# Kernel tuning notes

Measured on AMD Instinct MI355X. Metric: run time of the kernel, lower is better.

Reference implementation:

```python
import jax, jax.numpy as jnp
import numpy as np

B, NQ, N, D, H, R = 8, 64, 257, 768, 6, 64
DH = D // H  # 128
ALL_Q_MID = NQ * R  # 4096
LN_EPS = 1e-5


def setup_inputs() -> dict:
    key = jax.random.key(0)
    ks = jax.random.split(key, 7)
    s = 0.02
    return {
        "x": jax.random.normal(ks[0], (B, NQ, D), jnp.float32),
        "context": jax.random.normal(ks[1], (B, N, D), jnp.float32),
        "Wq": jax.random.normal(ks[2], (D, D), jnp.float32) * s,
        "Wk": jax.random.normal(ks[3], (D, D), jnp.float32) * s,
        "Wv1": jax.random.normal(ks[4], (ALL_Q_MID, D), jnp.float32) * s,
        "ln_g": jnp.ones((ALL_Q_MID,), jnp.float32),
        "ln_b": jnp.zeros((ALL_Q_MID,), jnp.float32),
        "Wconv": jax.random.normal(ks[5], (NQ, D, R), jnp.float32) * s,
        "Wout": jax.random.normal(ks[6], (D, D), jnp.float32) * s,
    }


def reference(x, context, Wq, Wk, Wv1, ln_g, ln_b, Wconv, Wout):
    b, nq, d = x.shape
    n = context.shape[1]
    dh = d // H

    # q, k projections, split heads: (b, h, len, dh)
    q = (x @ Wq.T).reshape(b, nq, H, dh).transpose(0, 2, 1, 3)
    k = (context @ Wk.T).reshape(b, n, H, dh).transpose(0, 2, 1, 3)

    # q-aware V: Linear -> LayerNorm(all_q_mid) -> grouped 1x1 conv (per-query lora expand)
    mid = context @ Wv1.T                                   # (b, n, NQ*R)
    mu = mid.mean(-1, keepdims=True)
    var = mid.var(-1, keepdims=True)
    mid = (mid - mu) * jax.lax.rsqrt(var + LN_EPS) * ln_g + ln_b
    midq = mid.reshape(b, n, NQ, -1)                        # (b, n, Q, r)
    v = jnp.einsum('bnqr,qdr->bqnd', midq, Wconv)           # per-query V: (b, Q, n, d)
    v = v.reshape(b, NQ, n, H, dh).transpose(0, 3, 1, 2, 4)  # (b, h, Q, n, dh)

    scale = dh ** (-0.25)
    sim = jnp.einsum('bhid,bhjd->bhij', q * scale, k * scale)  # (b, h, Q, n)
    attn = jax.nn.softmax(sim, axis=-1)
    # per-query value aggregation: attn[i, j] pairs with v[i, j, :]
    out = jnp.einsum('bhij,bhijd->bhid', attn, v)           # (b, h, Q, dh)
    out = out.transpose(0, 2, 1, 3).reshape(b, nq, d)       # (b, Q, d)
    return out @ Wout.T
```

## Files before the change

### kernel.cpp

```cpp
#include <hip/hip_runtime.h>

#define DEV __device__ __forceinline__

typedef __attribute__((ext_vector_type(8))) short sv8;
typedef __attribute__((ext_vector_type(4))) short sv4;
typedef __attribute__((ext_vector_type(4))) float f32x4;

DEV short f2bf(float f) {
  unsigned u = __float_as_uint(f);
  unsigned r = (u + 0x7fffu + ((u >> 16) & 1u)) >> 16;
  return (short)r;
}
DEV float bf2f(short s) {
  return __uint_as_float(((unsigned)(unsigned short)s) << 16);
}

DEV void gload16(const void* g, void* l) {
  __builtin_amdgcn_global_load_lds((const __attribute__((address_space(1))) void*)g,
                                   (__attribute__((address_space(3))) void*)l, 16, 0, 0);
}

__global__ __launch_bounds__(256) void fill_zero(float* __restrict__ p, int n4) {
  int i = blockIdx.x * 256 + threadIdx.x;
  if (i < n4) ((float4*)p)[i] = make_float4(0.f, 0.f, 0.f, 0.f);
}

struct CvtArgs {
  const float* s0; const float* s1; const float* s2;
  const float* s3; const float* s4; const float* s5;
  short* d0; short* d1; short* d2; short* d3; short* d4; short* d5;
  int e0, e1, e2, e3, e4, e5;
};
__global__ __launch_bounds__(256) void cvt_all(CvtArgs a) {
  int i = blockIdx.x * 256 + threadIdx.x;
  if (i >= a.e5) return;
  const float* s; short* d; int base;
  if      (i < a.e0) { s = a.s0; d = a.d0; base = 0; }
  else if (i < a.e1) { s = a.s1; d = a.d1; base = a.e0; }
  else if (i < a.e2) { s = a.s2; d = a.d2; base = a.e1; }
  else if (i < a.e3) { s = a.s3; d = a.d3; base = a.e2; }
  else if (i < a.e4) { s = a.s4; d = a.d4; base = a.e3; }
  else               { s = a.s5; d = a.d5; base = a.e4; }
  int j = i - base;
  float4 v = ((const float4*)s)[j];
  sv4 o = { f2bf(v.x), f2bf(v.y), f2bf(v.z), f2bf(v.w) };
  ((sv4*)d)[j] = o;
}

template <int MODE, int SPLITK>
DEV void gemm_tile(const short* __restrict__ A, const short* __restrict__ B,
                   void* __restrict__ C, int M, int N, int K,
                   int bm, int bn, int ks) {
  __shared__ __align__(16) short As[2][4096];
  __shared__ __align__(16) short Bs[2][4096];
  const int tid = threadIdx.x;
  const int wave = tid >> 6, lane = tid & 63;
  const int wr = wave >> 1, wc = wave & 1;
  const int row0 = bm * 128, col0 = bn * 128;
  const int rsel = lane & 15;
  const int Am = M - 1, Bm = N - 1;
  const int lr = lane >> 2;
  const int c8 = ((lane & 3) ^ ((lane >> 2) & 3)) * 8;
  const int Ksl = K / SPLITK;
  const int kbase = ks * Ksl;
  const int nt = Ksl / 32;

  const f32x4 z = {0.f, 0.f, 0.f, 0.f};
  f32x4 acc[4][4];
#pragma unroll
  for (int m = 0; m < 4; ++m)
#pragma unroll
    for (int n = 0; n < 4; ++n) acc[m][n] = z;

  auto stage = [&](int t, int buf) {
    int k0 = kbase + t * 32;
#pragma unroll
    for (int s = 0; s < 2; ++s) {
      int chunk = s * 4 + wave;
      int rr = chunk * 16 + lr;
      int gr = row0 + rr; if (gr > Am) gr = Am;
      gload16(A + (size_t)gr * K + k0 + c8, &As[buf][chunk * 512]);
      int gc = col0 + rr; if (gc > Bm) gc = Bm;
      gload16(B + (size_t)gc * K + k0 + c8, &Bs[buf][chunk * 512]);
    }
  };

  stage(0, 0);
  __syncthreads();
  const int ko = (((lane >> 4) ^ (rsel & 3)) * 8);

  for (int t = 0; t < nt; ++t) {
    int cur = t & 1;
    if (t + 1 < nt) stage(t + 1, cur ^ 1);
    sv8 a[4], b[4];
#pragma unroll
    for (int m = 0; m < 4; ++m)
      a[m] = *(const sv8*)(&As[cur][(wr * 64 + m * 16 + rsel) * 32 + ko]);
#pragma unroll
    for (int n = 0; n < 4; ++n)
      b[n] = *(const sv8*)(&Bs[cur][(wc * 64 + n * 16 + rsel) * 32 + ko]);
#pragma unroll
    for (int m = 0; m < 4; ++m)
#pragma unroll
      for (int n = 0; n < 4; ++n)
        acc[m][n] = __builtin_amdgcn_mfma_f32_16x16x32_bf16(a[m], b[n], acc[m][n], 0, 0, 0);
    __syncthreads();
  }

  const int cc = lane & 15, cr = (lane >> 4) * 4;
#pragma unroll
  for (int m = 0; m < 4; ++m)
#pragma unroll
    for (int n = 0; n < 4; ++n) {
      int c = col0 + wc * 64 + n * 16 + cc;
#pragma unroll
      for (int j = 0; j < 4; ++j) {
        int r = row0 + wr * 64 + m * 16 + cr + j;
        if (r < M && c < N) {
          float v = acc[m][n][j];
          if (MODE == 1)      ((short*)C)[(size_t)r * N + c] = f2bf(v);
          else if (MODE == 0) ((float*)C)[(size_t)r * N + c] = v;
          else                atomicAdd(&((float*)C)[(size_t)r * N + c], v);
        }
      }
    }
}

struct GSeg { const short* A; const short* B; short* C; int M; int nb; int blk0; };
__global__ __launch_bounds__(256) void gemm3(GSeg g0, GSeg g1, GSeg g2) {
  int bid = blockIdx.x;
  GSeg g;
  if (bid < g1.blk0) g = g0;
  else if (bid < g2.blk0) g = g1;
  else g = g2;
  int local = bid - g.blk0;
  int bm = local / g.nb, bn = local % g.nb;
  gemm_tile<1, 1>(g.A, g.B, g.C, g.M, g.nb * 128, 768, bm, bn, 0);
}

__global__ __launch_bounds__(256) void gemm_out_k(const short* __restrict__ A,
                                                  const short* __restrict__ B,
                                                  float* __restrict__ C) {
  gemm_tile<2, 4>(A, B, C, 512, 768, 768, blockIdx.x, blockIdx.y, blockIdx.z);
}

DEV void ln_body(int row, short* __restrict__ mid, const float* __restrict__ g,
                 const float* __restrict__ bb, float* rs, float* rss) {
  short* p = mid + (size_t)row * 4096;
  const int tid = threadIdx.x;
  sv8 v0 = *(const sv8*)(p + tid * 16);
  sv8 v1 = *(const sv8*)(p + tid * 16 + 8);
  float x[16];
#pragma unroll
  for (int j = 0; j < 8; ++j) { x[j] = bf2f(v0[j]); x[8 + j] = bf2f(v1[j]); }
  float s = 0.f, ss = 0.f;
#pragma unroll
  for (int j = 0; j < 16; ++j) { s += x[j]; ss += x[j] * x[j]; }
#pragma unroll
  for (int off = 32; off; off >>= 1) { s += __shfl_xor(s, off); ss += __shfl_xor(ss, off); }
  if ((tid & 63) == 0) { rs[tid >> 6] = s; rss[tid >> 6] = ss; }
  __syncthreads();
  float S = rs[0] + rs[1] + rs[2] + rs[3];
  float SS = rss[0] + rss[1] + rss[2] + rss[3];
  const float inv_n = 1.0f / 4096.0f;
  float mu = S * inv_n;
  float var = SS * inv_n - mu * mu;
  float rstd = rsqrtf(var + 1e-5f);
  const float4* g4 = (const float4*)(g + tid * 16);
  const float4* b4 = (const float4*)(bb + tid * 16);
  float y[16];
#pragma unroll
  for (int i = 0; i < 4; ++i) {
    float4 gg = g4[i], bv = b4[i];
    y[i * 4 + 0] = (x[i * 4 + 0] - mu) * rstd * gg.x + bv.x;
    y[i * 4 + 1] = (x[i * 4 + 1] - mu) * rstd * gg.y + bv.y;
    y[i * 4 + 2] = (x[i * 4 + 2] - mu) * rstd * gg.z + bv.z;
    y[i * 4 + 3] = (x[i * 4 + 3] - mu) * rstd * gg.w + bv.w;
  }
  sv8 o0, o1;
#pragma unroll
  for (int j = 0; j < 8; ++j) { o0[j] = f2bf(y[j]); o1[j] = f2bf(y[8 + j]); }
  *(sv8*)(p + tid * 16) = o0;
  *(sv8*)(p + tid * 16 + 8) = o1;
}

DEV void attn_body(int bh, const short* __restrict__ qb, const short* __restrict__ kb,
                   float* __restrict__ attn, float (*wred)[64]) {
  const int b = bh / 6, h = bh % 6;
  const int tid = threadIdx.x, wave = tid >> 6, lane = tid & 63;
  const int rsel = lane & 15, koff = (lane >> 4) * 8;
  const int rhi = (lane >> 4) * 4;

  const f32x4 z = {0.f, 0.f, 0.f, 0.f};
  f32x4 acc[4][5];
#pragma unroll
  for (int m = 0; m < 4; ++m)
#pragma unroll
    for (int i = 0; i < 5; ++i) acc[m][i] = z;

#pragma unroll
  for (int k0 = 0; k0 < 128; k0 += 32) {
    sv8 a[4];
#pragma unroll
    for (int m = 0; m < 4; ++m)
      a[m] = *(const sv8*)(qb + (size_t)(b * 64 + m * 16 + rsel) * 768 + h * 128 + k0 + koff);
#pragma unroll
    for (int i = 0; i < 5; ++i) {
      int nf = wave + i * 4;
      if (nf > 16) continue;
      int j = nf * 16 + rsel; if (j > 256) j = 256;
      sv8 bf = *(const sv8*)(kb + (size_t)(b * 257 + j) * 768 + h * 128 + k0 + koff);
#pragma unroll
      for (int m = 0; m < 4; ++m)
        acc[m][i] = __builtin_amdgcn_mfma_f32_16x16x32_bf16(a[m], bf, acc[m][i], 0, 0, 0);
    }
  }
  const float S2 = 0.08838834764831845f;
#pragma unroll
  for (int m = 0; m < 4; ++m)
#pragma unroll
    for (int i = 0; i < 5; ++i) {
      int col = (wave + i * 4) * 16 + rsel;
      bool valid = col < 257;
#pragma unroll
      for (int j = 0; j < 4; ++j)
        acc[m][i][j] = valid ? acc[m][i][j] * S2 : -1e30f;
    }
  float mx[4][4];
#pragma unroll
  for (int m = 0; m < 4; ++m)
#pragma unroll
    for (int j = 0; j < 4; ++j) {
      float pm = acc[m][0][j];
#pragma unroll
      for (int i = 1; i < 5; ++i) pm = fmaxf(pm, acc[m][i][j]);
      pm = fmaxf(pm, __shfl_xor(pm, 1));
      pm = fmaxf(pm, __shfl_xor(pm, 2));
      pm = fmaxf(pm, __shfl_xor(pm, 4));
      pm = fmaxf(pm, __shfl_xor(pm, 8));
      mx[m][j] = pm;
      if (rsel == 0) wred[wave][m * 16 + rhi + j] = pm;
    }
  __syncthreads();
#pragma unroll
  for (int m = 0; m < 4; ++m)
#pragma unroll
    for (int j = 0; j < 4; ++j) {
      int row = m * 16 + rhi + j;
      mx[m][j] = fmaxf(fmaxf(wred[0][row], wred[1][row]), fmaxf(wred[2][row], wred[3][row]));
    }
  __syncthreads();
  float inv[4][4];
#pragma unroll
  for (int m = 0; m < 4; ++m)
#pragma unroll
    for (int j = 0; j < 4; ++j) {
      float ps = 0.f;
#pragma unroll
      for (int i = 0; i < 5; ++i) {
        float e = __expf(acc[m][i][j] - mx[m][j]);
        acc[m][i][j] = e;
        ps += e;
      }
      ps += __shfl_xor(ps, 1);
      ps += __shfl_xor(ps, 2);
      ps += __shfl_xor(ps, 4);
      ps += __shfl_xor(ps, 8);
      if (rsel == 0) wred[wave][m * 16 + rhi + j] = ps;
    }
  __syncthreads();
  float* base = attn + (size_t)bh * 64 * 257;
#pragma unroll
  for (int m = 0; m < 4; ++m)
#pragma unroll
    for (int j = 0; j < 4; ++j) {
      int row = m * 16 + rhi + j;
      float tot = wred[0][row] + wred[1][row] + wred[2][row] + wred[3][row];
      inv[m][j] = 1.f / tot;
    }
#pragma unroll
  for (int m = 0; m < 4; ++m)
#pragma unroll
    for (int i = 0; i < 5; ++i) {
      int nf = wave + i * 4;
      if (nf > 16) continue;
      int col = nf * 16 + rsel;
      if (col < 257) {
#pragma unroll
        for (int j = 0; j < 4; ++j)
          base[(size_t)(m * 16 + rhi + j) * 257 + col] = acc[m][i][j] * inv[m][j];
      }
    }
}

__global__ __launch_bounds__(256) void ln_attn(short* __restrict__ mid,
                                               const float* __restrict__ g,
                                               const float* __restrict__ bb,
                                               const short* __restrict__ qb,
                                               const short* __restrict__ kb,
                                               float* __restrict__ attn) {
  __shared__ float wred[4][64];
  __shared__ float rs[4], rss[4];
  if (blockIdx.x < 48) attn_body(blockIdx.x, qb, kb, attn, wred);
  else                 ln_body(blockIdx.x - 48, mid, g, bb, rs, rss);
}

__global__ __launch_bounds__(256) void tk_kernel(const float* __restrict__ attn,
                                                 const short* __restrict__ mid,
                                                 float* __restrict__ t) {
  const int bq = blockIdx.x;
  const int b = bq >> 6, q = bq & 63;
  const int tid = threadIdx.x;
  __shared__ short ms[257][64];
  __shared__ float as_[6][257];
  for (int lin = tid; lin < 257 * 8; lin += 256) {
    int j = lin >> 3, seg = (lin & 7) * 8;
    *(sv8*)(&ms[j][seg]) = *(const sv8*)(mid + (size_t)(b * 257 + j) * 4096 + q * 64 + seg);
  }
#pragma unroll
  for (int h = 0; h < 6; ++h)
    for (int j = tid; j < 257; j += 256)
      as_[h][j] = attn[((size_t)(b * 6 + h) * 64 + q) * 257 + j];
  __syncthreads();
  for (int idx = tid; idx < 384; idx += 256) {
    int h = idx >> 6, r = idx & 63;
    float s = 0.f;
#pragma unroll 4
    for (int j = 0; j < 257; ++j) s += as_[h][j] * bf2f(ms[j][r]);
    t[((size_t)(b * 6 + h) * 64 + q) * 64 + r] = s;
  }
}

__global__ __launch_bounds__(256) void vproj_kernel(const float* __restrict__ t,
                                                    const float* __restrict__ Wconv,
                                                    short* __restrict__ op) {
  const int q = blockIdx.x, chunk = blockIdx.y;
  const int tid = threadIdx.x;
  __shared__ float ts[48][64];
  for (int lin = tid; lin < 48 * 64; lin += 256) {
    int bh = lin >> 6, r = lin & 63;
    ts[bh][r] = t[((size_t)bh * 64 + q) * 64 + r];
  }
  __syncthreads();
  const int d = chunk * 256 + tid;
  const int h = d >> 7;
  const float4* w4 = (const float4*)(Wconv + ((size_t)q * 768 + d) * 64);
  float acc[8] = {0.f, 0.f, 0.f, 0.f, 0.f, 0.f, 0.f, 0.f};
#pragma unroll
  for (int r4 = 0; r4 < 16; ++r4) {
    float4 w = w4[r4];
#pragma unroll
    for (int bb = 0; bb < 8; ++bb) {
      acc[bb] += w.x * ts[bb * 6 + h][r4 * 4 + 0];
      acc[bb] += w.y * ts[bb * 6 + h][r4 * 4 + 1];
      acc[bb] += w.z * ts[bb * 6 + h][r4 * 4 + 2];
      acc[bb] += w.w * ts[bb * 6 + h][r4 * 4 + 3];
    }
  }
#pragma unroll
  for (int bb = 0; bb < 8; ++bb)
    op[((size_t)(bb * 64 + q)) * 768 + d] = f2bf(acc[bb]);
}

extern "C" void kernel_launch(void* const* d_in, const int* in_sizes, int n_in,
                              void* d_out, int out_size, void* d_ws, size_t ws_size,
                              hipStream_t stream) {
  const float* x = (const float*)d_in[0];
  const float* ctx = (const float*)d_in[1];
  const float* Wq = (const float*)d_in[2];
  const float* Wk = (const float*)d_in[3];
  const float* Wv1 = (const float*)d_in[4];
  const float* ln_g = (const float*)d_in[5];
  const float* ln_b = (const float*)d_in[6];
  const float* Wconv = (const float*)d_in[7];
  const float* Wout = (const float*)d_in[8];
  float* out = (float*)d_out;
  (void)in_sizes; (void)n_in; (void)out_size; (void)ws_size;

  char* ws = (char*)d_ws;
  size_t off = 0;
  auto alloc = [&](size_t bytes) -> void* {
    void* p = (void*)(ws + off);
    off += (bytes + 255) & ~(size_t)255;
    return p;
  };
  short* x_bf    = (short*)alloc((size_t)393216 * 2);
  short* ctx_bf  = (short*)alloc((size_t)1579008 * 2);
  short* wq_bf   = (short*)alloc((size_t)589824 * 2);
  short* wk_bf   = (short*)alloc((size_t)589824 * 2);
  short* wv1_bf  = (short*)alloc((size_t)3145728 * 2);
  short* wout_bf = (short*)alloc((size_t)589824 * 2);
  short* q_bf    = (short*)alloc((size_t)393216 * 2);
  short* k_bf    = (short*)alloc((size_t)1579008 * 2);
  short* mid_bf  = (short*)alloc((size_t)8421376 * 2);
  float* attn    = (float*)alloc((size_t)789504 * 4);
  float* tbuf    = (float*)alloc((size_t)196608 * 4);
  short* op_bf   = (short*)alloc((size_t)393216 * 2);

  fill_zero<<<dim3(384), dim3(256), 0, stream>>>(out, 393216 / 4);

  CvtArgs ca;
  ca.s0 = x;   ca.d0 = x_bf;    int n0 = 393216 / 4;
  ca.s1 = ctx; ca.d1 = ctx_bf;  int n1 = 1579008 / 4;
  ca.s2 = Wq;  ca.d2 = wq_bf;   int n2 = 589824 / 4;
  ca.s3 = Wk;  ca.d3 = wk_bf;   int n3 = 589824 / 4;
  ca.s4 = Wv1; ca.d4 = wv1_bf;  int n4 = 3145728 / 4;
  ca.s5 = Wout; ca.d5 = wout_bf; int n5 = 589824 / 4;
  ca.e0 = n0; ca.e1 = ca.e0 + n1; ca.e2 = ca.e1 + n2;
  ca.e3 = ca.e2 + n3; ca.e4 = ca.e3 + n4; ca.e5 = ca.e4 + n5;
  cvt_all<<<dim3((ca.e5 + 255) / 256), dim3(256), 0, stream>>>(ca);

  GSeg s_q   = { x_bf,   wq_bf,  q_bf,   512,  6, 0 };
  GSeg s_k   = { ctx_bf, wk_bf,  k_bf,   2056, 6, 24 };
  GSeg s_mid = { ctx_bf, wv1_bf, mid_bf, 2056, 32, 126 };
  gemm3<<<dim3(670), dim3(256), 0, stream>>>(s_q, s_k, s_mid);

  ln_attn<<<dim3(2104), dim3(256), 0, stream>>>(mid_bf, ln_g, ln_b, q_bf, k_bf, attn);

  tk_kernel<<<dim3(512), dim3(256), 0, stream>>>(attn, mid_bf, tbuf);

  vproj_kernel<<<dim3(64, 3), dim3(256), 0, stream>>>(tbuf, Wconv, op_bf);

  gemm_out_k<<<dim3(4, 6, 4), dim3(256), 0, stream>>>(op_bf, wout_bf, out);
}
```

Baseline: 183.5 us.

## Fuse all stages into a persistent cooperative megakernel with grid syncs

Replaces the chain of separate kernel launches (zero-fill, convert, projection GEMMs, layernorm/attention, tk, vproj, output GEMM) with one cooperative persistent kernel that loops over work items per phase and separates phases with grid-wide syncs. The output GEMM changes from atomic split-K into a zeroed buffer to an 8-way split-K writing partial buffers, followed by a reduction phase, which removes the fill and the atomics. The aim is to cut launch gaps and per-kernel ramp-up. In exchange it adds grid barrier costs, limits the grid to the number of co-resident blocks (occupancy capped at 2 blocks per CU with about 39KB of LDS each), and keeps a multi-kernel fallback path.

```diff
diff --git a/kernel.cpp b/kernel.cpp
--- a/kernel.cpp
+++ b/kernel.cpp
@@ -1,4 +1,7 @@
 #include <hip/hip_runtime.h>
+#include <hip/hip_cooperative_groups.h>
+
+namespace cg = cooperative_groups;
 
 #define DEV __device__ __forceinline__
 
@@ -20,39 +23,20 @@
                                    (__attribute__((address_space(3))) void*)l, 16, 0, 0);
 }
 
-__global__ __launch_bounds__(256) void fill_zero(float* __restrict__ p, int n4) {
-  int i = blockIdx.x * 256 + threadIdx.x;
-  if (i < n4) ((float4*)p)[i] = make_float4(0.f, 0.f, 0.f, 0.f);
-}
-
-struct CvtArgs {
-  const float* s0; const float* s1; const float* s2;
-  const float* s3; const float* s4; const float* s5;
-  short* d0; short* d1; short* d2; short* d3; short* d4; short* d5;
-  int e0, e1, e2, e3, e4, e5;
+struct MegaArgs {
+  const float *x, *ctx, *Wq, *Wk, *Wv1, *ln_g, *ln_b, *Wconv, *Wout;
+  short *x_bf, *ctx_bf, *wq_bf, *wk_bf, *wv1_bf, *wout_bf;
+  short *q_bf, *k_bf, *mid_bf, *op_bf;
+  float *attn, *tbuf, *part, *out;
 };
-__global__ __launch_bounds__(256) void cvt_all(CvtArgs a) {
-  int i = blockIdx.x * 256 + threadIdx.x;
-  if (i >= a.e5) return;
-  const float* s; short* d; int base;
-  if      (i < a.e0) { s = a.s0; d = a.d0; base = 0; }
-  else if (i < a.e1) { s = a.s1; d = a.d1; base = a.e0; }
-  else if (i < a.e2) { s = a.s2; d = a.d2; base = a.e1; }
-  else if (i < a.e3) { s = a.s3; d = a.d3; base = a.e2; }
-  else if (i < a.e4) { s = a.s4; d = a.d4; base = a.e3; }
-  else               { s = a.s5; d = a.d5; base = a.e4; }
-  int j = i - base;
-  float4 v = ((const float4*)s)[j];
-  sv4 o = { f2bf(v.x), f2bf(v.y), f2bf(v.z), f2bf(v.w) };
-  ((sv4*)d)[j] = o;
-}
+
 
 template <int MODE, int SPLITK>
-DEV void gemm_tile(const short* __restrict__ A, const short* __restrict__ B,
+DEV void gemm_tile(char* smem, const short* __restrict__ A, const short* __restrict__ B,
                    void* __restrict__ C, int M, int N, int K,
                    int bm, int bn, int ks) {
-  __shared__ __align__(16) short As[2][4096];
-  __shared__ __align__(16) short Bs[2][4096];
+  short* As = (short*)smem;
+  short* Bs = As + 8192;
   const int tid = threadIdx.x;
   const int wave = tid >> 6, lane = tid & 63;
   const int wr = wave >> 1, wc = wave & 1;
@@ -79,9 +63,9 @@
       int chunk = s * 4 + wave;
       int rr = chunk * 16 + lr;
       int gr = row0 + rr; if (gr > Am) gr = Am;
-      gload16(A + (size_t)gr * K + k0 + c8, &As[buf][chunk * 512]);
+      gload16(A + (size_t)gr * K + k0 + c8, As + buf * 4096 + chunk * 512);
       int gc = col0 + rr; if (gc > Bm) gc = Bm;
-      gload16(B + (size_t)gc * K + k0 + c8, &Bs[buf][chunk * 512]);
+      gload16(B + (size_t)gc * K + k0 + c8, Bs + buf * 4096 + chunk * 512);
     }
   };
 
@@ -95,10 +79,10 @@
     sv8 a[4], b[4];
 #pragma unroll
     for (int m = 0; m < 4; ++m)
-      a[m] = *(const sv8*)(&As[cur][(wr * 64 + m * 16 + rsel) * 32 + ko]);
+      a[m] = *(const sv8*)(As + cur * 4096 + (wr * 64 + m * 16 + rsel) * 32 + ko);
 #pragma unroll
     for (int n = 0; n < 4; ++n)
-      b[n] = *(const sv8*)(&Bs[cur][(wc * 64 + n * 16 + rsel) * 32 + ko]);
+      b[n] = *(const sv8*)(Bs + cur * 4096 + (wc * 64 + n * 16 + rsel) * 32 + ko);
 #pragma unroll
     for (int m = 0; m < 4; ++m)
 #pragma unroll
@@ -118,34 +102,17 @@
         int r = row0 + wr * 64 + m * 16 + cr + j;
         if (r < M && c < N) {
           float v = acc[m][n][j];
-          if (MODE == 1)      ((short*)C)[(size_t)r * N + c] = f2bf(v);
-          else if (MODE == 0) ((float*)C)[(size_t)r * N + c] = v;
-          else                atomicAdd(&((float*)C)[(size_t)r * N + c], v);
+          if (MODE == 1) ((short*)C)[(size_t)r * N + c] = f2bf(v);
+          else           ((float*)C)[(size_t)r * N + c] = v;
         }
       }
     }
 }
 
-struct GSeg { const short* A; const short* B; short* C; int M; int nb; int blk0; };
-__global__ __launch_bounds__(256) void gemm3(GSeg g0, GSeg g1, GSeg g2) {
-  int bid = blockIdx.x;
-  GSeg g;
-  if (bid < g1.blk0) g = g0;
-  else if (bid < g2.blk0) g = g1;
-  else g = g2;
-  int local = bid - g.blk0;
-  int bm = local / g.nb, bn = local % g.nb;
-  gemm_tile<1, 1>(g.A, g.B, g.C, g.M, g.nb * 128, 768, bm, bn, 0);
-}
-
-__global__ __launch_bounds__(256) void gemm_out_k(const short* __restrict__ A,
-                                                  const short* __restrict__ B,
-                                                  float* __restrict__ C) {
-  gemm_tile<2, 4>(A, B, C, 512, 768, 768, blockIdx.x, blockIdx.y, blockIdx.z);
-}
-
 DEV void ln_body(int row, short* __restrict__ mid, const float* __restrict__ g,
-                 const float* __restrict__ bb, float* rs, float* rss) {
+                 const float* __restrict__ bb, char* smem) {
+  float* rs = (float*)smem;
+  float* rss = rs + 4;
   short* p = mid + (size_t)row * 4096;
   const int tid = threadIdx.x;
   sv8 v0 = *(const sv8*)(p + tid * 16);
@@ -162,6 +129,7 @@
   __syncthreads();
   float S = rs[0] + rs[1] + rs[2] + rs[3];
   float SS = rss[0] + rss[1] + rss[2] + rss[3];
+  __syncthreads();
   const float inv_n = 1.0f / 4096.0f;
   float mu = S * inv_n;
   float var = SS * inv_n - mu * mu;
@@ -185,7 +153,8 @@
 }
 
 DEV void attn_body(int bh, const short* __restrict__ qb, const short* __restrict__ kb,
-                   float* __restrict__ attn, float (*wred)[64]) {
+                   float* __restrict__ attn, char* smem) {
+  float (*wred)[64] = (float(*)[64])smem;
   const int b = bh / 6, h = bh % 6;
   const int tid = threadIdx.x, wave = tid >> 6, lane = tid & 63;
   const int rsel = lane & 15, koff = (lane >> 4) * 8;
@@ -278,6 +247,7 @@
       float tot = wred[0][row] + wred[1][row] + wred[2][row] + wred[3][row];
       inv[m][j] = 1.f / tot;
     }
+  __syncthreads();
 #pragma unroll
   for (int m = 0; m < 4; ++m)
 #pragma unroll
@@ -293,26 +263,12 @@
     }
 }
 
-__global__ __launch_bounds__(256) void ln_attn(short* __restrict__ mid,
-                                               const float* __restrict__ g,
-                                               const float* __restrict__ bb,
-                                               const short* __restrict__ qb,
-                                               const short* __restrict__ kb,
-                                               float* __restrict__ attn) {
-  __shared__ float wred[4][64];
-  __shared__ float rs[4], rss[4];
-  if (blockIdx.x < 48) attn_body(blockIdx.x, qb, kb, attn, wred);
-  else                 ln_body(blockIdx.x - 48, mid, g, bb, rs, rss);
-}
-
-__global__ __launch_bounds__(256) void tk_kernel(const float* __restrict__ attn,
-                                                 const short* __restrict__ mid,
-                                                 float* __restrict__ t) {
-  const int bq = blockIdx.x;
+DEV void tk_body(int bq, char* smem, const float* __restrict__ attn,
+                 const short* __restrict__ mid, float* __restrict__ t) {
+  short (*ms)[64] = (short(*)[64])smem;
+  float (*as_)[257] = (float(*)[257])(smem + 32896);
   const int b = bq >> 6, q = bq & 63;
   const int tid = threadIdx.x;
-  __shared__ short ms[257][64];
-  __shared__ float as_[6][257];
   for (int lin = tid; lin < 257 * 8; lin += 256) {
     int j = lin >> 3, seg = (lin & 7) * 8;
     *(sv8*)(&ms[j][seg]) = *(const sv8*)(mid + (size_t)(b * 257 + j) * 4096 + q * 64 + seg);
@@ -329,14 +285,13 @@
     for (int j = 0; j < 257; ++j) s += as_[h][j] * bf2f(ms[j][r]);
     t[((size_t)(b * 6 + h) * 64 + q) * 64 + r] = s;
   }
-}
-
-__global__ __launch_bounds__(256) void vproj_kernel(const float* __restrict__ t,
-                                                    const float* __restrict__ Wconv,
-                                                    short* __restrict__ op) {
-  const int q = blockIdx.x, chunk = blockIdx.y;
+  __syncthreads();
+}
+
+DEV void vproj_body(int q, int chunk, char* smem, const float* __restrict__ t,
+                    const float* __restrict__ Wconv, short* __restrict__ op) {
+  float (*ts)[64] = (float(*)[64])smem;
   const int tid = threadIdx.x;
-  __shared__ float ts[48][64];
   for (int lin = tid; lin < 48 * 64; lin += 256) {
     int bh = lin >> 6, r = lin & 63;
     ts[bh][r] = t[((size_t)bh * 64 + q) * 64 + r];
@@ -360,21 +315,105 @@
 #pragma unroll
   for (int bb = 0; bb < 8; ++bb)
     op[((size_t)(bb * 64 + q)) * 768 + d] = f2bf(acc[bb]);
+  __syncthreads();
+}
+
+DEV void phaseA(const MegaArgs& a, int gtid, int T) {
+  for (int i = gtid; i < 1721856; i += T) {
+    const float* s; short* d; int base;
+    if      (i < 98304)   { s = a.x;    d = a.x_bf;    base = 0; }
+    else if (i < 493056)  { s = a.ctx;  d = a.ctx_bf;  base = 98304; }
+    else if (i < 640512)  { s = a.Wq;   d = a.wq_bf;   base = 493056; }
+    else if (i < 787968)  { s = a.Wk;   d = a.wk_bf;   base = 640512; }
+    else if (i < 1574400) { s = a.Wv1;  d = a.wv1_bf;  base = 787968; }
+    else                  { s = a.Wout; d = a.wout_bf; base = 1574400; }
+    int j = i - base;
+    float4 v = ((const float4*)s)[j];
+    sv4 o = { f2bf(v.x), f2bf(v.y), f2bf(v.z), f2bf(v.w) };
+    ((sv4*)d)[j] = o;
+  }
+}
+DEV void phaseB(const MegaArgs& a, char* smem, int tile) {
+  const short *A_, *B_; short* C_; int M_, nb_, local;
+  if (tile < 24)       { A_ = a.x_bf;   B_ = a.wq_bf;  C_ = a.q_bf;   M_ = 512;  nb_ = 6;  local = tile; }
+  else if (tile < 126) { A_ = a.ctx_bf; B_ = a.wk_bf;  C_ = a.k_bf;   M_ = 2056; nb_ = 6;  local = tile - 24; }
+  else                 { A_ = a.ctx_bf; B_ = a.wv1_bf; C_ = a.mid_bf; M_ = 2056; nb_ = 32; local = tile - 126; }
+  gemm_tile<1, 1>(smem, A_, B_, C_, M_, nb_ * 128, 768, local / nb_, local % nb_, 0);
+}
+DEV void phaseC(const MegaArgs& a, char* smem, int item) {
+  if (item < 48) attn_body(item, a.q_bf, a.k_bf, a.attn, smem);
+  else           ln_body(item - 48, a.mid_bf, a.ln_g, a.ln_b, smem);
+}
+DEV void phaseF(const MegaArgs& a, char* smem, int it) {
+  int ks = it & 7, t24 = it >> 3;
+  gemm_tile<0, 8>(smem, a.op_bf, a.wout_bf, a.part + (size_t)ks * 393216,
+                  512, 768, 768, t24 & 3, t24 >> 2, ks);
+}
+DEV void phaseG(const MegaArgs& a, int gtid, int T) {
+  for (int i = gtid; i < 98304; i += T) {
+    float4 s = ((const float4*)a.part)[i];
+#pragma unroll
+    for (int k = 1; k < 8; ++k) {
+      float4 p = ((const float4*)(a.part + (size_t)k * 393216))[i];
+      s.x += p.x; s.y += p.y; s.z += p.z; s.w += p.w;
+    }
+    ((float4*)a.out)[i] = s;
+  }
+}
+
+__global__ __launch_bounds__(256, 2) void mega(MegaArgs a) {
+  __shared__ __align__(16) char smem[39104];
+  cg::grid_group grid = cg::this_grid();
+  const int bid = blockIdx.x, tid = threadIdx.x;
+  const int G = gridDim.x;
+  const int gtid = bid * 256 + tid;
+  const int T = G * 256;
+
+  phaseA(a, gtid, T);
+  __threadfence(); grid.sync(); __threadfence();
+  for (int tile = bid; tile < 670; tile += G) phaseB(a, smem, tile);
+  __threadfence(); grid.sync(); __threadfence();
+  for (int item = bid; item < 2104; item += G) phaseC(a, smem, item);
+  __threadfence(); grid.sync(); __threadfence();
+  for (int bq = bid; bq < 512; bq += G) tk_body(bq, smem, a.attn, a.mid_bf, a.tbuf);
+  __threadfence(); grid.sync(); __threadfence();
+  for (int it = bid; it < 192; it += G) vproj_body(it / 3, it % 3, smem, a.tbuf, a.Wconv, a.op_bf);
+  __threadfence(); grid.sync(); __threadfence();
+  for (int it = bid; it < 192; it += G) phaseF(a, smem, it);
+  __threadfence(); grid.sync(); __threadfence();
+  phaseG(a, gtid, T);
+}
+
+__global__ __launch_bounds__(256) void k_cvt(MegaArgs a) {
+  phaseA(a, blockIdx.x * 256 + threadIdx.x, gridDim.x * 256);
+}
+__global__ __launch_bounds__(256) void k_gemm3(MegaArgs a) {
+  __shared__ __align__(16) char smem[16384];
+  phaseB(a, smem, blockIdx.x);
+}
+__global__ __launch_bounds__(256) void k_lnattn(MegaArgs a) {
+  __shared__ __align__(16) char smem[1024];
+  phaseC(a, smem, blockIdx.x);
+}
+__global__ __launch_bounds__(256) void k_tk(MegaArgs a) {
+  __shared__ __align__(16) char smem[39104];
+  tk_body(blockIdx.x, smem, a.attn, a.mid_bf, a.tbuf);
+}
+__global__ __launch_bounds__(256) void k_vproj(MegaArgs a) {
+  __shared__ __align__(16) char smem[12288];
+  vproj_body(blockIdx.x / 3, blockIdx.x % 3, smem, a.tbuf, a.Wconv, a.op_bf);
+}
+__global__ __launch_bounds__(256) void k_outk(MegaArgs a) {
+  __shared__ __align__(16) char smem[16384];
+  phaseF(a, smem, blockIdx.x);
+}
+__global__ __launch_bounds__(256) void k_red(MegaArgs a) {
+  phaseG(a, blockIdx.x * 256 + threadIdx.x, gridDim.x * 256);
 }
 
 extern "C" void kernel_launch(void* const* d_in, const int* in_sizes, int n_in,
                               void* d_out, int out_size, void* d_ws, size_t ws_size,
                               hipStream_t stream) {
-  const float* x = (const float*)d_in[0];
-  const float* ctx = (const float*)d_in[1];
-  const float* Wq = (const float*)d_in[2];
-  const float* Wk = (const float*)d_in[3];
-  const float* Wv1 = (const float*)d_in[4];
-  const float* ln_g = (const float*)d_in[5];
-  const float* ln_b = (const float*)d_in[6];
-  const float* Wconv = (const float*)d_in[7];
-  const float* Wout = (const float*)d_in[8];
-  float* out = (float*)d_out;
   (void)in_sizes; (void)n_in; (void)out_size; (void)ws_size;
 
   char* ws = (char*)d_ws;
@@ -384,42 +423,54 @@
     off += (bytes + 255) & ~(size_t)255;
     return p;
   };
-  short* x_bf    = (short*)alloc((size_t)393216 * 2);
-  short* ctx_bf  = (short*)alloc((size_t)1579008 * 2);
-  short* wq_bf   = (short*)alloc((size_t)589824 * 2);
-  short* wk_bf   = (short*)alloc((size_t)589824 * 2);
-  short* wv1_bf  = (short*)alloc((size_t)3145728 * 2);
-  short* wout_bf = (short*)alloc((size_t)589824 * 2);
-  short* q_bf    = (short*)alloc((size_t)393216 * 2);
-  short* k_bf    = (short*)alloc((size_t)1579008 * 2);
-  short* mid_bf  = (short*)alloc((size_t)8421376 * 2);
-  float* attn    = (float*)alloc((size_t)789504 * 4);
-  float* tbuf    = (float*)alloc((size_t)196608 * 4);
-  short* op_bf   = (short*)alloc((size_t)393216 * 2);
-
-  fill_zero<<<dim3(384), dim3(256), 0, stream>>>(out, 393216 / 4);
-
-  CvtArgs ca;
-  ca.s0 = x;   ca.d0 = x_bf;    int n0 = 393216 / 4;
-  ca.s1 = ctx; ca.d1 = ctx_bf;  int n1 = 1579008 / 4;
-  ca.s2 = Wq;  ca.d2 = wq_bf;   int n2 = 589824 / 4;
-  ca.s3 = Wk;  ca.d3 = wk_bf;   int n3 = 589824 / 4;
-  ca.s4 = Wv1; ca.d4 = wv1_bf;  int n4 = 3145728 / 4;
-  ca.s5 = Wout; ca.d5 = wout_bf; int n5 = 589824 / 4;
-  ca.e0 = n0; ca.e1 = ca.e0 + n1; ca.e2 = ca.e1 + n2;
-  ca.e3 = ca.e2 + n3; ca.e4 = ca.e3 + n4; ca.e5 = ca.e4 + n5;
-  cvt_all<<<dim3((ca.e5 + 255) / 256), dim3(256), 0, stream>>>(ca);
-
-  GSeg s_q   = { x_bf,   wq_bf,  q_bf,   512,  6, 0 };
-  GSeg s_k   = { ctx_bf, wk_bf,  k_bf,   2056, 6, 24 };
-  GSeg s_mid = { ctx_bf, wv1_bf, mid_bf, 2056, 32, 126 };
-  gemm3<<<dim3(670), dim3(256), 0, stream>>>(s_q, s_k, s_mid);
-
-  ln_attn<<<dim3(2104), dim3(256), 0, stream>>>(mid_bf, ln_g, ln_b, q_bf, k_bf, attn);
-
-  tk_kernel<<<dim3(512), dim3(256), 0, stream>>>(attn, mid_bf, tbuf);
-
-  vproj_kernel<<<dim3(64, 3), dim3(256), 0, stream>>>(tbuf, Wconv, op_bf);
-
-  gemm_out_k<<<dim3(4, 6, 4), dim3(256), 0, stream>>>(op_bf, wout_bf, out);
-}
+
+  MegaArgs a;
+  a.x    = (const float*)d_in[0];
+  a.ctx  = (const float*)d_in[1];
+  a.Wq   = (const float*)d_in[2];
+  a.Wk   = (const float*)d_in[3];
+  a.Wv1  = (const float*)d_in[4];
+  a.ln_g = (const float*)d_in[5];
+  a.ln_b = (const float*)d_in[6];
+  a.Wconv = (const float*)d_in[7];
+  a.Wout = (const float*)d_in[8];
+  a.out  = (float*)d_out;
+
+  a.x_bf    = (short*)alloc((size_t)393216 * 2);
+  a.ctx_bf  = (short*)alloc((size_t)1579008 * 2);
+  a.wq_bf   = (short*)alloc((size_t)589824 * 2);
+  a.wk_bf   = (short*)alloc((size_t)589824 * 2);
+  a.wv1_bf  = (short*)alloc((size_t)3145728 * 2);
+  a.wout_bf = (short*)alloc((size_t)589824 * 2);
+  a.q_bf    = (short*)alloc((size_t)393216 * 2);
+  a.k_bf    = (short*)alloc((size_t)1579008 * 2);
+  a.mid_bf  = (short*)alloc((size_t)8421376 * 2);
+  a.attn    = (float*)alloc((size_t)789504 * 4);
+  a.tbuf    = (float*)alloc((size_t)196608 * 4);
+  a.op_bf   = (short*)alloc((size_t)393216 * 2);
+  a.part    = (float*)alloc((size_t)393216 * 8 * 4);
+
+  int dev = 0;
+  (void)hipGetDevice(&dev);
+  int ncu = 256;
+  if (hipDeviceGetAttribute(&ncu, hipDeviceAttributeMultiprocessorCount, dev) != hipSuccess || ncu <= 0)
+    ncu = 256;
+  int occ = 0;
+  int grid = 256;
+  if (hipOccupancyMaxActiveBlocksPerMultiprocessor(&occ, (const void*)mega, 256, 0) == hipSuccess && occ >= 1)
+    grid = occ * ncu;
+  if (grid > 768) grid = 768;
+
+  void* kargs[] = { (void*)&a };
+  hipError_t le = hipLaunchCooperativeKernel((const void*)mega, dim3(grid), dim3(256),
+                                             kargs, 0, stream);
+  if (le != hipSuccess) {
+    k_cvt<<<dim3(2048), dim3(256), 0, stream>>>(a);
+    k_gemm3<<<dim3(670), dim3(256), 0, stream>>>(a);
+    k_lnattn<<<dim3(2104), dim3(256), 0, stream>>>(a);
+    k_tk<<<dim3(512), dim3(256), 0, stream>>>(a);
+    k_vproj<<<dim3(192), dim3(256), 0, stream>>>(a);
+    k_outk<<<dim3(192), dim3(256), 0, stream>>>(a);
+    k_red<<<dim3(384), dim3(256), 0, stream>>>(a);
+  }
+}
```

Measured after the change: 664.9 us. +262.3%, slower.
